# Optimization experiments

Measured on AMD Instinct MI355X. Metric: run time of the kernel, lower is better.

The kernel has to match this reference:

```python
import jax, jax.numpy as jnp
import numpy as np

B, S, H, NH = 2, 2048, 1024, 16
P = H // NH

def setup_inputs() -> dict:
    key = jax.random.key(0)
    k1, k2, k3, k4 = jax.random.split(key, 4)
    x = jax.random.normal(k1, (B, S, H), dtype=jnp.float32)
    mask = jax.random.randint(k2, (B, S), 0, 2).astype(jnp.int32)
    # weights: (num_heads, 3, hidden, partial) -- the leading singleton dim of the
    # torch parameter is pure broadcast, dropped here.
    W = jax.random.normal(k3, (NH, 3, H, P), dtype=jnp.float32) * (1.0 / np.sqrt(H))
    Wl = jax.random.normal(k4, (H, H), dtype=jnp.float32) * (1.0 / np.sqrt(H))
    bl = jnp.zeros((H,), dtype=jnp.float32)
    return {"x": x, "mask": mask, "W": W, "Wl": Wl, "bl": bl}

def reference(x, mask, W, Wl, bl):
    nh, _, h, p = W.shape
    scale = 1.0 / np.sqrt(p)
    # kvq[b, t, n, s, p]; t=0 keys, t=1 values, t=2 queries (unbind order in source)
    kvq = jnp.einsum('bsh,nthp->btnsp', x, W)
    keys, values, queries = kvq[:, 0], kvq[:, 1], kvq[:, 2]  # each [B, NH, S, P]
    # NOTE: source computes keys @ queries^T -> scores[b,n,i,j] = k_i . q_j
    scores = jnp.einsum('bnip,bnjp->bnij', keys, queries) * scale
    # mask==0 zeroes out the LAST axis (query positions), exactly as the fancy-index write
    scores = jnp.where(mask[:, None, None, :] == 0, jnp.float32(-1e12), scores)
    # softmax over dim=2 (key axis), as in the source (Softmax(dim=2))
    w = jax.nn.softmax(scores, axis=2)
    out = jnp.einsum('bnij,bnjp->bnip', w, values)  # [B, NH, S, P]
    b, _, s, _ = out.shape
    hidden = out.transpose(0, 2, 1, 3).reshape(b, s, nh * p)  # concat heads
    return hidden @ Wl.T + bl
```

## Files before the change

kernel.cpp:

```cpp
#include <hip/hip_runtime.h>

#define B_ 2
#define S_ 2048
#define H_ 1024
#define NH_ 16
#define P_ 64

using f32x4 = __attribute__((ext_vector_type(4))) float;
using i32x4 = __attribute__((ext_vector_type(4))) int;
using f16   = _Float16;
using f16x8 = __attribute__((ext_vector_type(8))) f16;
using f16x4 = __attribute__((ext_vector_type(4))) f16;
using h16x2 = __attribute__((ext_vector_type(2))) __fp16;

#define QSCALE 0.18033688f

static __device__ __forceinline__ f16x8 ldh8(const f16* p) { return *(const f16x8*)p; }
static __device__ __forceinline__ f16x4 ldh4(const f16* p) { return *(const f16x4*)p; }
static __device__ __forceinline__ f32x4 ld4f(const float* p) { return *(const f32x4*)p; }

static __device__ __forceinline__ f32x4 mm16(f16x8 a, f16x8 b, f32x4 c) {
  return __builtin_amdgcn_mfma_f32_16x16x32_f16(a, b, c, 0, 0, 0);
}

__global__ __launch_bounds__(256) void prep_kernel(
    const float* __restrict__ W, const float* __restrict__ Wl,
    f16* __restrict__ WtH, f16* __restrict__ WlH)
{
  __shared__ float T[64 * 65];
  const int tid = threadIdx.x;
  if (blockIdx.x < 768) {
    const int nt = blockIdx.x >> 4;
    const int h0 = (blockIdx.x & 15) * 64;
    const float* src = W + (size_t)nt * H_ * P_ + (size_t)h0 * P_;
    #pragma unroll
    for (int r = 0; r < 4; ++r) {
      int idx = tid + r * 256;
      int h = idx >> 4, p4 = (idx & 15) << 2;
      f32x4 v = ld4f(src + (size_t)h * P_ + p4);
      #pragma unroll
      for (int i = 0; i < 4; ++i) T[(p4 + i) * 65 + h] = v[i];
    }
    __syncthreads();
    f16* dh = WtH + (size_t)nt * P_ * H_;
    #pragma unroll
    for (int r = 0; r < 4; ++r) {
      int idx = tid + r * 256;
      int p = idx >> 4, h4 = (idx & 15) << 2;
      f16x4 hv;
      #pragma unroll
      for (int i = 0; i < 4; ++i) hv[i] = (f16)T[p * 65 + h4 + i];
      *(f16x4*)(dh + (size_t)p * H_ + h0 + h4) = hv;
    }
  } else {
    int idx = (blockIdx.x - 768) * 256 + tid;
    f32x4 v = ((const f32x4*)Wl)[idx];
    f16x4 h;
    #pragma unroll
    for (int i = 0; i < 4; ++i) h[i] = (f16)v[i];
    ((f16x4*)WlH)[idx] = h;
  }
}

__global__ __launch_bounds__(256) void qkv_kernel(
    const float* __restrict__ x, const f16* __restrict__ WtH,
    f16* __restrict__ Kh, f16* __restrict__ Qh, f16* __restrict__ VTh)
{
  __shared__ f16 xls[2][64 * 64];

  int blk = blockIdx.x;
  const int st = blk & 31; blk >>= 5;
  const int n = blk & 15;
  const int b = blk >> 4;
  const int s0 = st * 64;
  const int tid = threadIdx.x;
  const int w = tid >> 6, lane = tid & 63, q = lane >> 4, fr = lane & 15;
  const int bn = b * NH_ + n;

  const int srow = tid >> 2, scc = tid & 3;
  const float* xsrc = x + ((size_t)b * S_ + s0 + srow) * H_ + 16 * scc;
  const int c0 = ((2 * scc) ^ (srow & 7)) * 8;
  const int c1 = ((2 * scc + 1) ^ (srow & 7)) * 8;

  auto stage = [&](int k0, int bs) {
    f32x4 v0 = ld4f(xsrc + k0),     v1 = ld4f(xsrc + k0 + 4);
    f32x4 v2 = ld4f(xsrc + k0 + 8), v3 = ld4f(xsrc + k0 + 12);
    f16x8 a, b2;
    #pragma unroll
    for (int e = 0; e < 4; ++e) {
      a[e] = (f16)v0[e];  a[e + 4] = (f16)v1[e];
      b2[e] = (f16)v2[e]; b2[e + 4] = (f16)v3[e];
    }
    *(f16x8*)&xls[bs][srow * 64 + c0] = a;
    *(f16x8*)&xls[bs][srow * 64 + c1] = b2;
  };

  const f16* WtK = WtH + ((size_t)(n * 3 + 0) * P_ + 16 * w + fr) * H_ + 8 * q;
  const f16* WtV = WtH + ((size_t)(n * 3 + 1) * P_ + 16 * w + fr) * H_ + 8 * q;
  const f16* WtQ = WtH + ((size_t)(n * 3 + 2) * P_ + 16 * w + fr) * H_ + 8 * q;

  f32x4 accK[4] = {}, accQ[4] = {}, accV[4] = {};

  stage(0, 0);
  for (int step = 0; step < 16; ++step) {
    __syncthreads();
    if (step < 15) stage((step + 1) * 64, (step + 1) & 1);
    const int bs = step & 1;
    const int k0 = step * 64;

    f16x8 xf[4][2];
    #pragma unroll
    for (int ss = 0; ss < 4; ++ss) {
      int row = 16 * ss + fr;
      #pragma unroll
      for (int ks = 0; ks < 2; ++ks) {
        int ch = ((q + 4 * ks) ^ (row & 7)) * 8;
        xf[ss][ks] = *(const f16x8*)&xls[bs][row * 64 + ch];
      }
    }
    f16x8 wk0 = ldh8(WtK + k0), wk1 = ldh8(WtK + k0 + 32);
    f16x8 wq0 = ldh8(WtQ + k0), wq1 = ldh8(WtQ + k0 + 32);
    f16x8 wv0 = ldh8(WtV + k0), wv1 = ldh8(WtV + k0 + 32);
    #pragma unroll
    for (int ss = 0; ss < 4; ++ss) {
      accK[ss] = mm16(wk0, xf[ss][0], accK[ss]);
      accK[ss] = mm16(wk1, xf[ss][1], accK[ss]);
      accQ[ss] = mm16(wq0, xf[ss][0], accQ[ss]);
      accQ[ss] = mm16(wq1, xf[ss][1], accQ[ss]);
      accV[ss] = mm16(xf[ss][0], wv0, accV[ss]);
      accV[ss] = mm16(xf[ss][1], wv1, accV[ss]);
    }
  }

  #pragma unroll
  for (int ss = 0; ss < 4; ++ss) {
    f16x4 hK, hQ;
    #pragma unroll
    for (int c = 0; c < 4; ++c) {
      hK[c] = (f16)accK[ss][c];
      hQ[c] = (f16)(accQ[ss][c] * QSCALE);
    }
    size_t off = ((size_t)bn * S_ + (s0 + 16 * ss + fr)) * P_ + 16 * w + 4 * q;
    *(f16x4*)(Kh + off) = hK;
    *(f16x4*)(Qh + off) = hQ;
  }
  #pragma unroll
  for (int ss = 0; ss < 4; ++ss) {
    f16x4 hV;
    #pragma unroll
    for (int c = 0; c < 4; ++c) hV[c] = (f16)accV[ss][c];
    size_t off = ((size_t)bn * P_ + (16 * w + fr)) * S_ + s0 + 16 * ss + 4 * q;
    *(f16x4*)(VTh + off) = hV;
  }
}

__global__ __launch_bounds__(256) void stats_kernel(
    const f16* __restrict__ Kh, const f16* __restrict__ Qh,
    f16* __restrict__ VT, const int* __restrict__ mask,
    float* __restrict__ Cbuf)
{
  __shared__ float zbuf[2 * 128];
  const int tid = threadIdx.x;
  const int bid = blockIdx.x;
  const int j0 = (bid & 15) * 128;
  const int bn = bid >> 4;
  const int w = tid >> 6, lane = tid & 63, q = lane >> 4, fr = lane & 15;
  const int jb = 64 * (w & 1), ih = w >> 1, ib0 = 32 * ih;

  f16x8 qf[4][2];
  #pragma unroll
  for (int jt = 0; jt < 4; ++jt)
    #pragma unroll
    for (int ks = 0; ks < 2; ++ks)
      qf[jt][ks] = ldh8(Qh + ((size_t)bn * S_ + (j0 + jb + 16 * jt + fr)) * P_ + 8 * q + 32 * ks);

  f32x4 z[4] = {};
  f16x8 kA[2][2], kB[2][2];

  auto loadK = [&](f16x8 (&kf)[2][2], int i0) {
    #pragma unroll
    for (int it = 0; it < 2; ++it)
      #pragma unroll
      for (int ks = 0; ks < 2; ++ks)
        kf[it][ks] = ldh8(Kh + ((size_t)bn * S_ + (i0 + ib0 + 16 * it + fr)) * P_ + 8 * q + 32 * ks);
  };
  auto step = [&](f16x8 (&kf)[2][2]) {
    f32x4 sc[4][2] = {};
    __builtin_amdgcn_s_setprio(1);
    #pragma unroll
    for (int ks = 0; ks < 2; ++ks)
      #pragma unroll
      for (int jt = 0; jt < 4; ++jt)
        #pragma unroll
        for (int it = 0; it < 2; ++it)
          sc[jt][it] = mm16(qf[jt][ks], kf[it][ks], sc[jt][it]);
    __builtin_amdgcn_s_setprio(0);
    #pragma unroll
    for (int jt = 0; jt < 4; ++jt)
      #pragma unroll
      for (int c = 0; c < 4; ++c)
        z[jt][c] += exp2f(sc[jt][0][c]) + exp2f(sc[jt][1][c]);
  };

  loadK(kA, 0);
  for (int i0 = 0; i0 < S_; i0 += 128) {
    loadK(kB, i0 + 64);
    step(kA);
    loadK(kA, (i0 + 128) & (S_ - 1));
    step(kB);
  }

  #pragma unroll
  for (int msk = 1; msk <= 8; msk <<= 1)
    #pragma unroll
    for (int jt = 0; jt < 4; ++jt)
      #pragma unroll
      for (int c = 0; c < 4; ++c)
        z[jt][c] += __shfl_xor(z[jt][c], msk, 64);

  if (fr == 0) {
    #pragma unroll
    for (int jt = 0; jt < 4; ++jt)
      *(f32x4*)&zbuf[ih * 128 + jb + 16 * jt + 4 * q] = z[jt];
  }
  __syncthreads();
  if (tid < 128)
    zbuf[tid] = 1.0f / (zbuf[tid] + zbuf[128 + tid]);
  __syncthreads();

  const int sp = tid >> 2;
  const int jc = (tid & 3) * 32;
  f16* vrow = VT + ((size_t)bn * P_ + sp) * S_ + j0 + jc;
  const int* mr = mask + (size_t)(bn >> 4) * S_ + j0 + jc;
  float acc = 0.0f;
  #pragma unroll
  for (int k = 0; k < 4; ++k) {
    f16x8 v = *(const f16x8*)(vrow + 8 * k);
    f16x8 o;
    #pragma unroll
    for (int e = 0; e < 8; ++e) {
      float fv = (float)v[e];
      if (mr[8 * k + e] != 0) o[e] = (f16)(fv * zbuf[jc + 8 * k + e]);
      else { o[e] = (f16)0.0f; acc += fv; }
    }
    *(f16x8*)(vrow + 8 * k) = o;
  }
  acc += __shfl_xor(acc, 1, 64);
  acc += __shfl_xor(acc, 2, 64);
  if ((tid & 3) == 0) atomicAdd(&Cbuf[bn * P_ + sp], acc * (1.0f / S_));
}

__global__ __launch_bounds__(256) void av_kernel(
    const f16* __restrict__ Kh, const f16* __restrict__ Qh,
    const f16* __restrict__ VT, const float* __restrict__ Cbuf,
    f16* __restrict__ hidh)
{
  __shared__ __align__(16) float accl[64 * 68];
  const int tid = threadIdx.x;
  const int bid = blockIdx.x;
  const int i0 = (bid & 31) * 64;
  const int bn = bid >> 5;
  const int b = bn >> 4, n = bn & 15;
  const int w = tid >> 6, lane = tid & 63, q = lane >> 4, fr = lane & 15;

  f16x8 kf[4][2];
  #pragma unroll
  for (int it = 0; it < 4; ++it)
    #pragma unroll
    for (int ks = 0; ks < 2; ++ks)
      kf[it][ks] = ldh8(Kh + ((size_t)bn * S_ + (i0 + 16 * it + fr)) * P_ + 8 * q + 32 * ks);

  const f16* qp = Qh + ((size_t)bn * S_ + (w * 32 + fr)) * P_ + 8 * q;
  const f16* vp = VT + ((size_t)bn * P_ + fr) * S_ + w * 32 + 4 * q;

  f32x4 opv[4][4] = {};

  for (int T = 0; T < 16; ++T) {
    f16x8 aq00 = ldh8(qp);
    f16x8 aq01 = ldh8(qp + 32);
    f16x8 aq10 = ldh8(qp + 1024);
    f16x8 aq11 = ldh8(qp + 1056);
    f16x8 va[4];
    #pragma unroll
    for (int pt = 0; pt < 4; ++pt) {
      union { f16x8 v8; f16x4 h4[2]; } u;
      u.h4[0] = ldh4(vp + (size_t)(16 * pt) * S_);
      u.h4[1] = ldh4(vp + (size_t)(16 * pt) * S_ + 16);
      va[pt] = u.v8;
    }
    qp += 128 * 64;
    vp += 128;

    #pragma unroll
    for (int it = 0; it < 4; ++it) {
      f32x4 s0 = {}, s1 = {};
      s0 = mm16(aq00, kf[it][0], s0);
      s0 = mm16(aq01, kf[it][1], s0);
      s1 = mm16(aq10, kf[it][0], s1);
      s1 = mm16(aq11, kf[it][1], s1);
      union { f16x8 v8; h16x2 h[4]; } ef;
      ef.h[0] = __builtin_amdgcn_cvt_pkrtz(exp2f(s0[0]), exp2f(s0[1]));
      ef.h[1] = __builtin_amdgcn_cvt_pkrtz(exp2f(s0[2]), exp2f(s0[3]));
      ef.h[2] = __builtin_amdgcn_cvt_pkrtz(exp2f(s1[0]), exp2f(s1[1]));
      ef.h[3] = __builtin_amdgcn_cvt_pkrtz(exp2f(s1[2]), exp2f(s1[3]));
      opv[0][it] = mm16(va[0], ef.v8, opv[0][it]);
      opv[1][it] = mm16(va[1], ef.v8, opv[1][it]);
      opv[2][it] = mm16(va[2], ef.v8, opv[2][it]);
      opv[3][it] = mm16(va[3], ef.v8, opv[3][it]);
    }
  }

  #pragma unroll
  for (int r = 0; r < 4; ++r) {
    __syncthreads();
    if (w == r) {
      #pragma unroll
      for (int it = 0; it < 4; ++it)
        #pragma unroll
        for (int pt = 0; pt < 4; ++pt) {
          float* a = &accl[(16 * it + fr) * 68 + 16 * pt + 4 * q];
          if (r == 0) *(f32x4*)a = opv[pt][it];
          else {
            f32x4 old = *(const f32x4*)a;
            #pragma unroll
            for (int c = 0; c < 4; ++c) old[c] += opv[pt][it][c];
            *(f32x4*)a = old;
          }
        }
    }
  }
  __syncthreads();

  const int ti = tid >> 2;
  const int tp = (tid & 3) << 4;
  const float* cb = Cbuf + bn * P_ + tp;
  f16* dst = hidh + ((size_t)b * S_ + (i0 + ti)) * H_ + n * P_ + tp;
  #pragma unroll
  for (int h = 0; h < 2; ++h) {
    f32x4 a0 = *(const f32x4*)&accl[ti * 68 + tp + 8 * h];
    f32x4 a1 = *(const f32x4*)&accl[ti * 68 + tp + 8 * h + 4];
    f32x4 c0 = ld4f(cb + 8 * h);
    f32x4 c1 = ld4f(cb + 8 * h + 4);
    f16x8 o;
    #pragma unroll
    for (int e = 0; e < 4; ++e) {
      o[e]     = (f16)(a0[e] + c0[e]);
      o[e + 4] = (f16)(a1[e] + c1[e]);
    }
    *(f16x8*)(dst + 8 * h) = o;
  }
}

__global__ __launch_bounds__(256) void final_kernel(
    const f16* __restrict__ hidh, const f16* __restrict__ WlH,
    const float* __restrict__ bl, float* __restrict__ out)
{
  __shared__ f16 hl[2][64 * 64];
  const int tid = threadIdx.x;
  const int ot = blockIdx.x & 15;
  const int rt = blockIdx.x >> 4;
  const int r0 = rt * 64, o0 = ot * 64;
  const int w = tid >> 6, lane = tid & 63, q = lane >> 4, fr = lane & 15;

  const int srow = tid >> 2, scc = tid & 3;
  const f16* hsrc = hidh + (size_t)(r0 + srow) * H_ + 16 * scc;
  const int c0 = ((2 * scc) ^ (srow & 7)) * 8;
  const int c1 = ((2 * scc + 1) ^ (srow & 7)) * 8;

  auto stage = [&](int k0, int bs) {
    f16x8 a = ldh8(hsrc + k0);
    f16x8 b2 = ldh8(hsrc + k0 + 8);
    *(f16x8*)&hl[bs][srow * 64 + c0] = a;
    *(f16x8*)&hl[bs][srow * 64 + c1] = b2;
  };

  const f16* WlA = WlH + ((size_t)(o0 + 16 * w + fr)) * H_ + 8 * q;

  f32x4 acc[4] = {};

  stage(0, 0);
  for (int step = 0; step < 16; ++step) {
    __syncthreads();
    if (step < 15) stage((step + 1) * 64, (step + 1) & 1);
    const int bs = step & 1;
    const int k0 = step * 64;

    f16x8 bh[4][2];
    #pragma unroll
    for (int ss = 0; ss < 4; ++ss) {
      int row = 16 * ss + fr;
      #pragma unroll
      for (int ks = 0; ks < 2; ++ks) {
        int ch = ((q + 4 * ks) ^ (row & 7)) * 8;
        bh[ss][ks] = *(const f16x8*)&hl[bs][row * 64 + ch];
      }
    }
    f16x8 ah0 = ldh8(WlA + k0);
    f16x8 ah1 = ldh8(WlA + k0 + 32);
    #pragma unroll
    for (int ss = 0; ss < 4; ++ss) {
      acc[ss] = mm16(ah0, bh[ss][0], acc[ss]);
      acc[ss] = mm16(ah1, bh[ss][1], acc[ss]);
    }
  }

  const int o = o0 + 16 * w + 4 * q;
  f32x4 bv = ld4f(bl + o);
  #pragma unroll
  for (int ss = 0; ss < 4; ++ss) {
    f32x4 v;
    #pragma unroll
    for (int c = 0; c < 4; ++c) v[c] = acc[ss][c] + bv[c];
    *(f32x4*)(out + (size_t)(r0 + 16 * ss + fr) * H_ + o) = v;
  }
}

extern "C" void kernel_launch(void* const* d_in, const int* in_sizes, int n_in,
                              void* d_out, int out_size, void* d_ws, size_t ws_size,
                              hipStream_t stream) {
  const float* x    = (const float*)d_in[0];
  const int*   mask = (const int*)d_in[1];
  const float* W    = (const float*)d_in[2];
  const float* Wl   = (const float*)d_in[3];
  const float* bl   = (const float*)d_in[4];
  float* out = (float*)d_out;

  const size_t SZ  = (size_t)B_ * NH_ * S_ * P_;
  const size_t SZW = (size_t)NH_ * 3 * H_ * P_;
  const size_t SZL = (size_t)H_ * H_;
  const size_t SZH = (size_t)B_ * S_ * H_;

  char* p = (char*)d_ws;
  f16*   Kh   = (f16*)p;  p += SZ * 2;
  f16*   Qh   = (f16*)p;  p += SZ * 2;
  f16*   VTh  = (f16*)p;  p += SZ * 2;
  f16*   WtH  = (f16*)p;  p += SZW * 2;
  f16*   WlH  = (f16*)p;  p += SZL * 2;
  f16*   hidh = (f16*)p;  p += SZH * 2;
  float* Cbuf = (float*)p; p += (size_t)B_ * NH_ * P_ * 4;

  prep_kernel <<<1792, 256, 0, stream>>>(W, Wl, WtH, WlH);
  qkv_kernel  <<<B_ * NH_ * (S_ / 64), 256, 0, stream>>>(x, WtH, Kh, Qh, VTh);
  hipMemsetAsync(Cbuf, 0, (size_t)B_ * NH_ * P_ * 4, stream);
  stats_kernel<<<B_ * NH_ * (S_ / 128), 256, 0, stream>>>(
      Kh, Qh, VTh, mask, Cbuf);
  av_kernel   <<<B_ * NH_ * (S_ / 64), 256, 0, stream>>>(
      Kh, Qh, VTh, Cbuf, hidh);
  final_kernel<<<(B_ * S_ / 64) * (H_ / 64), 256, 0, stream>>>(
      hidh, WlH, bl, out);
}
```

Measured before the change: 241.3 us.

## Stage exp scores through LDS to enable contiguous 8-wide V loads in av kernel

In the attention-value kernel, each wave now writes its exponentiated score fragments to a per-wave LDS scratch and reads them back in a transposed layout. This lets V be loaded as one contiguous 16-byte load per tile instead of two strided 8-byte loads, and it overlaps the PV MFMAs for the previous tile with the score computation for the current one. The shared buffer is reused for the final accumulation. Separately, the normalisation kernel reads the mask as vector int4 loads. The change adds LDS traffic and relies on intra-wave ordering without explicit barriers.

After: 215.5 us. 1.12x faster.

```diff
diff --git a/kernel.cpp b/kernel.cpp
--- a/kernel.cpp
+++ b/kernel.cpp
@@ -16,7 +16,6 @@
 #define QSCALE 0.18033688f
 
 static __device__ __forceinline__ f16x8 ldh8(const f16* p) { return *(const f16x8*)p; }
-static __device__ __forceinline__ f16x4 ldh4(const f16* p) { return *(const f16x4*)p; }
 static __device__ __forceinline__ f32x4 ld4f(const float* p) { return *(const f32x4*)p; }
 
 static __device__ __forceinline__ f32x4 mm16(f16x8 a, f16x8 b, f32x4 c) {
@@ -236,12 +235,17 @@
   #pragma unroll
   for (int k = 0; k < 4; ++k) {
     f16x8 v = *(const f16x8*)(vrow + 8 * k);
+    i32x4 m0 = *(const i32x4*)(mr + 8 * k);
+    i32x4 m1 = *(const i32x4*)(mr + 8 * k + 4);
     f16x8 o;
     #pragma unroll
-    for (int e = 0; e < 8; ++e) {
+    for (int e = 0; e < 4; ++e) {
       float fv = (float)v[e];
-      if (mr[8 * k + e] != 0) o[e] = (f16)(fv * zbuf[jc + 8 * k + e]);
+      if (m0[e] != 0) o[e] = (f16)(fv * zbuf[jc + 8 * k + e]);
       else { o[e] = (f16)0.0f; acc += fv; }
+      float fv2 = (float)v[e + 4];
+      if (m1[e] != 0) o[e + 4] = (f16)(fv2 * zbuf[jc + 8 * k + e + 4]);
+      else { o[e + 4] = (f16)0.0f; acc += fv2; }
     }
     *(f16x8*)(vrow + 8 * k) = o;
   }
@@ -255,13 +259,14 @@
     const f16* __restrict__ VT, const float* __restrict__ Cbuf,
     f16* __restrict__ hidh)
 {
-  __shared__ __align__(16) float accl[64 * 68];
+  __shared__ __align__(16) char smem[18432];
   const int tid = threadIdx.x;
   const int bid = blockIdx.x;
   const int i0 = (bid & 31) * 64;
   const int bn = bid >> 5;
   const int b = bn >> 4, n = bn & 15;
   const int w = tid >> 6, lane = tid & 63, q = lane >> 4, fr = lane & 15;
+  f16* ew = (f16*)smem + w * (64 * 36);
 
   f16x8 kf[4][2];
   #pragma unroll
@@ -270,8 +275,11 @@
     for (int ks = 0; ks < 2; ++ks)
       kf[it][ks] = ldh8(Kh + ((size_t)bn * S_ + (i0 + 16 * it + fr)) * P_ + 8 * q + 32 * ks);
 
-  const f16* qp = Qh + ((size_t)bn * S_ + (w * 32 + fr)) * P_ + 8 * q;
-  const f16* vp = VT + ((size_t)bn * P_ + fr) * S_ + w * 32 + 4 * q;
+  const f16* qp  = Qh + ((size_t)bn * S_ + (w * 32 + fr)) * P_ + 8 * q;
+  const f16* vp0 = VT + ((size_t)bn * P_ + fr) * S_ + w * 32 + 8 * q;
+  const f16* vp1 = vp0 + (size_t)16 * S_;
+  const f16* vp2 = vp0 + (size_t)32 * S_;
+  const f16* vp3 = vp0 + (size_t)48 * S_;
 
   f32x4 opv[4][4] = {};
 
@@ -280,36 +288,45 @@
     f16x8 aq01 = ldh8(qp + 32);
     f16x8 aq10 = ldh8(qp + 1024);
     f16x8 aq11 = ldh8(qp + 1056);
-    f16x8 va[4];
-    #pragma unroll
-    for (int pt = 0; pt < 4; ++pt) {
-      union { f16x8 v8; f16x4 h4[2]; } u;
-      u.h4[0] = ldh4(vp + (size_t)(16 * pt) * S_);
-      u.h4[1] = ldh4(vp + (size_t)(16 * pt) * S_ + 16);
-      va[pt] = u.v8;
-    }
+    f16x8 va0 = ldh8(vp0), va1 = ldh8(vp1), va2 = ldh8(vp2), va3 = ldh8(vp3);
     qp += 128 * 64;
-    vp += 128;
+    vp0 += 128; vp1 += 128; vp2 += 128; vp3 += 128;
 
     #pragma unroll
     for (int it = 0; it < 4; ++it) {
-      f32x4 s0 = {}, s1 = {};
-      s0 = mm16(aq00, kf[it][0], s0);
-      s0 = mm16(aq01, kf[it][1], s0);
-      s1 = mm16(aq10, kf[it][0], s1);
-      s1 = mm16(aq11, kf[it][1], s1);
-      union { f16x8 v8; h16x2 h[4]; } ef;
-      ef.h[0] = __builtin_amdgcn_cvt_pkrtz(exp2f(s0[0]), exp2f(s0[1]));
-      ef.h[1] = __builtin_amdgcn_cvt_pkrtz(exp2f(s0[2]), exp2f(s0[3]));
-      ef.h[2] = __builtin_amdgcn_cvt_pkrtz(exp2f(s1[0]), exp2f(s1[1]));
-      ef.h[3] = __builtin_amdgcn_cvt_pkrtz(exp2f(s1[2]), exp2f(s1[3]));
-      opv[0][it] = mm16(va[0], ef.v8, opv[0][it]);
-      opv[1][it] = mm16(va[1], ef.v8, opv[1][it]);
-      opv[2][it] = mm16(va[2], ef.v8, opv[2][it]);
-      opv[3][it] = mm16(va[3], ef.v8, opv[3][it]);
-    }
-  }
-
+      {
+        f32x4 s0 = {}, s1 = {};
+        s0 = mm16(aq00, kf[it][0], s0);
+        s0 = mm16(aq01, kf[it][1], s0);
+        s1 = mm16(aq10, kf[it][0], s1);
+        s1 = mm16(aq11, kf[it][1], s1);
+        union { f16x4 v; h16x2 h[2]; } e0, e1;
+        e0.h[0] = __builtin_amdgcn_cvt_pkrtz(exp2f(s0[0]), exp2f(s0[1]));
+        e0.h[1] = __builtin_amdgcn_cvt_pkrtz(exp2f(s0[2]), exp2f(s0[3]));
+        e1.h[0] = __builtin_amdgcn_cvt_pkrtz(exp2f(s1[0]), exp2f(s1[1]));
+        e1.h[1] = __builtin_amdgcn_cvt_pkrtz(exp2f(s1[2]), exp2f(s1[3]));
+        *(f16x4*)(ew + (16 * it + fr) * 36 + 4 * q)      = e0.v;
+        *(f16x4*)(ew + (16 * it + fr) * 36 + 16 + 4 * q) = e1.v;
+      }
+      if (it > 0) {
+        const int pv = it - 1;
+        f16x8 ef = *(const f16x8*)(ew + (16 * pv + fr) * 36 + 8 * q);
+        opv[0][pv] = mm16(va0, ef, opv[0][pv]);
+        opv[1][pv] = mm16(va1, ef, opv[1][pv]);
+        opv[2][pv] = mm16(va2, ef, opv[2][pv]);
+        opv[3][pv] = mm16(va3, ef, opv[3][pv]);
+      }
+    }
+    {
+      f16x8 ef = *(const f16x8*)(ew + (16 * 3 + fr) * 36 + 8 * q);
+      opv[0][3] = mm16(va0, ef, opv[0][3]);
+      opv[1][3] = mm16(va1, ef, opv[1][3]);
+      opv[2][3] = mm16(va2, ef, opv[2][3]);
+      opv[3][3] = mm16(va3, ef, opv[3][3]);
+    }
+  }
+
+  float* accl = (float*)smem;
   #pragma unroll
   for (int r = 0; r < 4; ++r) {
     __syncthreads();
```

## Permute stored V layout so attention kernel loads V fragments with single 16-byte reads

Applied to the files above, without the earlier changes.

The normalization kernel now writes each 32-element V chunk in a permuted order that matches the MFMA operand layout, and it loads the mask as int4 vectors instead of scalar reads. The AV kernel can then fetch each V fragment with one 8-half load per row block instead of two 4-half loads. This reduces the number of memory instructions in the hot loop. In exchange, the producer and consumer become coupled through an implicit permuted layout and the producer uses a 32-element register staging array.

Result: faster. 214.3 us (-11.2%).

```diff
diff --git a/kernel.cpp b/kernel.cpp
--- a/kernel.cpp
+++ b/kernel.cpp
@@ -16,7 +16,6 @@
 #define QSCALE 0.18033688f
 
 static __device__ __forceinline__ f16x8 ldh8(const f16* p) { return *(const f16x8*)p; }
-static __device__ __forceinline__ f16x4 ldh4(const f16* p) { return *(const f16x4*)p; }
 static __device__ __forceinline__ f32x4 ld4f(const float* p) { return *(const f32x4*)p; }
 
 static __device__ __forceinline__ f32x4 mm16(f16x8 a, f16x8 b, f32x4 c) {
@@ -233,17 +232,31 @@
   f16* vrow = VT + ((size_t)bn * P_ + sp) * S_ + j0 + jc;
   const int* mr = mask + (size_t)(bn >> 4) * S_ + j0 + jc;
   float acc = 0.0f;
+  f16 lo[32];
   #pragma unroll
   for (int k = 0; k < 4; ++k) {
     f16x8 v = *(const f16x8*)(vrow + 8 * k);
+    i32x4 m0 = *(const i32x4*)(mr + 8 * k);
+    i32x4 m1 = *(const i32x4*)(mr + 8 * k + 4);
+    #pragma unroll
+    for (int e = 0; e < 4; ++e) {
+      float fv = (float)v[e];
+      if (m0[e] != 0) lo[8 * k + e] = (f16)(fv * zbuf[jc + 8 * k + e]);
+      else { lo[8 * k + e] = (f16)0.0f; acc += fv; }
+      float fv2 = (float)v[e + 4];
+      if (m1[e] != 0) lo[8 * k + e + 4] = (f16)(fv2 * zbuf[jc + 8 * k + e + 4]);
+      else { lo[8 * k + e + 4] = (f16)0.0f; acc += fv2; }
+    }
+  }
+  #pragma unroll
+  for (int k2 = 0; k2 < 4; ++k2) {
     f16x8 o;
     #pragma unroll
     for (int e = 0; e < 8; ++e) {
-      float fv = (float)v[e];
-      if (mr[8 * k + e] != 0) o[e] = (f16)(fv * zbuf[jc + 8 * k + e]);
-      else { o[e] = (f16)0.0f; acc += fv; }
-    }
-    *(f16x8*)(vrow + 8 * k) = o;
+      const int l = 4 * k2 + (e & 3) + ((e & 4) ? 16 : 0);
+      o[e] = lo[l];
+    }
+    *(f16x8*)(vrow + 8 * k2) = o;
   }
   acc += __shfl_xor(acc, 1, 64);
   acc += __shfl_xor(acc, 2, 64);
@@ -270,8 +283,11 @@
     for (int ks = 0; ks < 2; ++ks)
       kf[it][ks] = ldh8(Kh + ((size_t)bn * S_ + (i0 + 16 * it + fr)) * P_ + 8 * q + 32 * ks);
 
-  const f16* qp = Qh + ((size_t)bn * S_ + (w * 32 + fr)) * P_ + 8 * q;
-  const f16* vp = VT + ((size_t)bn * P_ + fr) * S_ + w * 32 + 4 * q;
+  const f16* qp  = Qh + ((size_t)bn * S_ + (w * 32 + fr)) * P_ + 8 * q;
+  const f16* vp0 = VT + ((size_t)bn * P_ + fr) * S_ + w * 32 + 8 * q;
+  const f16* vp1 = vp0 + (size_t)16 * S_;
+  const f16* vp2 = vp0 + (size_t)32 * S_;
+  const f16* vp3 = vp0 + (size_t)48 * S_;
 
   f32x4 opv[4][4] = {};
 
@@ -280,16 +296,9 @@
     f16x8 aq01 = ldh8(qp + 32);
     f16x8 aq10 = ldh8(qp + 1024);
     f16x8 aq11 = ldh8(qp + 1056);
-    f16x8 va[4];
-    #pragma unroll
-    for (int pt = 0; pt < 4; ++pt) {
-      union { f16x8 v8; f16x4 h4[2]; } u;
-      u.h4[0] = ldh4(vp + (size_t)(16 * pt) * S_);
-      u.h4[1] = ldh4(vp + (size_t)(16 * pt) * S_ + 16);
-      va[pt] = u.v8;
-    }
+    f16x8 va0 = ldh8(vp0), va1 = ldh8(vp1), va2 = ldh8(vp2), va3 = ldh8(vp3);
     qp += 128 * 64;
-    vp += 128;
+    vp0 += 128; vp1 += 128; vp2 += 128; vp3 += 128;
 
     #pragma unroll
     for (int it = 0; it < 4; ++it) {
@@ -303,10 +312,10 @@
       ef.h[1] = __builtin_amdgcn_cvt_pkrtz(exp2f(s0[2]), exp2f(s0[3]));
       ef.h[2] = __builtin_amdgcn_cvt_pkrtz(exp2f(s1[0]), exp2f(s1[1]));
       ef.h[3] = __builtin_amdgcn_cvt_pkrtz(exp2f(s1[2]), exp2f(s1[3]));
-      opv[0][it] = mm16(va[0], ef.v8, opv[0][it]);
-      opv[1][it] = mm16(va[1], ef.v8, opv[1][it]);
-      opv[2][it] = mm16(va[2], ef.v8, opv[2][it]);
-      opv[3][it] = mm16(va[3], ef.v8, opv[3][it]);
+      opv[0][it] = mm16(va0, ef.v8, opv[0][it]);
+      opv[1][it] = mm16(va1, ef.v8, opv[1][it]);
+      opv[2][it] = mm16(va2, ef.v8, opv[2][it]);
+      opv[3][it] = mm16(va3, ef.v8, opv[3][it]);
     }
   }
 
```
